# Optimization experiments

Hardware: AMD Instinct MI355X
Metric: run time of the kernel (lower is better)

Reference implementation:

```python
import jax, jax.numpy as jnp
import numpy as np

B, S, HID = 1, 2048, 4096
NH, NKV = 32, 8
HD = HID // NH            # 128
GROUPS = NH // NKV        # 4
ROPE_THETA = 10000.0


def _rope_cos_sin(seq_len, head_dim, dtype=jnp.float32):
    inv_freq = 1.0 / (ROPE_THETA ** (jnp.arange(0, head_dim, 2, dtype=jnp.float32) / head_dim))
    t = jnp.arange(seq_len, dtype=jnp.float32)
    freqs = jnp.outer(t, inv_freq)                      # [S, HD/2]
    emb = jnp.concatenate([freqs, freqs], axis=-1)      # [S, HD]
    return jnp.cos(emb).astype(dtype), jnp.sin(emb).astype(dtype)


def _rotate_half(x):
    x1, x2 = jnp.split(x, 2, axis=-1)
    return jnp.concatenate([-x2, x1], axis=-1)


def _apply_rope(x, cos, sin):
    # x: [B, H, S, HD]; cos/sin: [S, HD] (position_ids = arange(S), no past)
    return x * cos[None, None] + _rotate_half(x) * sin[None, None]


def setup_inputs() -> dict:
    key = jax.random.key(0)
    k1, k2, k3, k4, k5 = jax.random.split(key, 5)
    return {
        "hidden_states": jax.random.normal(k1, (B, S, HID), jnp.float32),
        "Wq": jax.random.normal(k2, (NH * HD, HID), jnp.float32) * 0.02,
        "Wk": jax.random.normal(k3, (NKV * HD, HID), jnp.float32) * 0.02,
        "Wv": jax.random.normal(k4, (NKV * HD, HID), jnp.float32) * 0.02,
        "Wo": jax.random.normal(k5, (HID, NH * HD), jnp.float32) * 0.02,
    }


def reference(hidden_states, Wq, Wk, Wv, Wo):
    bsz, q_len, _ = hidden_states.shape
    # projections (nn.Linear: x @ W.T)
    q = (hidden_states @ Wq.T).reshape(bsz, q_len, NH, HD).transpose(0, 2, 1, 3)   # [B,NH,S,HD]
    k = (hidden_states @ Wk.T).reshape(bsz, q_len, NKV, HD).transpose(0, 2, 1, 3)  # [B,NKV,S,HD]
    v = (hidden_states @ Wv.T).reshape(bsz, q_len, NKV, HD).transpose(0, 2, 1, 3)

    cos, sin = _rope_cos_sin(q_len, HD, hidden_states.dtype)
    q = _apply_rope(q, cos, sin)
    k = _apply_rope(k, cos, sin)

    # GQA: repeat kv heads (repeat_kv / num_key_value_groups)
    k = jnp.repeat(k, GROUPS, axis=1)   # [B,NH,S,HD]
    v = jnp.repeat(v, GROUPS, axis=1)

    scale = 1.0 / jnp.sqrt(jnp.asarray(HD, hidden_states.dtype))
    logits = jnp.einsum('bhqd,bhkd->bhqk', q, k) * scale   # [B,NH,S,S]

    # prefill causal mask (phys_past_len = 0)
    causal = jnp.tril(jnp.ones((q_len, q_len), dtype=bool))
    logits = jnp.where(causal[None, None], logits, jnp.finfo(logits.dtype).min)

    attn = jax.nn.softmax(logits, axis=-1)
    out = jnp.einsum('bhqk,bhkd->bhqd', attn, v)            # [B,NH,S,HD]
    out = out.transpose(0, 2, 1, 3).reshape(bsz, q_len, NH * HD)
    return out @ Wo.T
```

## Files before the change

kernel.cpp:

```cpp
#include <hip/hip_runtime.h>

typedef __bf16 bf16;
typedef __bf16 bf16x4 __attribute__((ext_vector_type(4)));
typedef __bf16 bf16x8 __attribute__((ext_vector_type(8)));
typedef float f32x4 __attribute__((ext_vector_type(4)));

#define S_LEN 2048
#define HID_DIM 4096
#define NH 32
#define NKV 8
#define HD 128
#define QKV_N 6144
#define K_COL 4096
#define V_COL 5120
#define PADV 76

__global__ void cvt_all_kernel(const float* __restrict__ hs, const float* __restrict__ wq,
                               const float* __restrict__ wk, const float* __restrict__ wv,
                               const float* __restrict__ wo, bf16* __restrict__ hsb,
                               bf16* __restrict__ wqkvb, bf16* __restrict__ wob) {
  long i = (long)blockIdx.x * blockDim.x + threadIdx.x;
  const float* src; bf16* dst; long off;
  if (i < 2097152)      { src = hs; dst = hsb;   off = i; }
  else if (i < 6291456) { src = wq; dst = wqkvb; off = i - 2097152; }
  else if (i < 7340032) { src = wk; dst = wqkvb + (long)4096 * 4096 / 4 * 4; off = i - 6291456; dst = wqkvb + (long)4096 * 4096; }
  else if (i < 8388608) { src = wv; dst = wqkvb + (long)5120 * 4096; off = i - 7340032; }
  else                  { src = wo; dst = wob;   off = i - 8388608; }
  float4 v = reinterpret_cast<const float4*>(src)[off];
  bf16x4 o;
  o[0] = (bf16)v.x; o[1] = (bf16)v.y; o[2] = (bf16)v.z; o[3] = (bf16)v.w;
  reinterpret_cast<bf16x4*>(dst)[off] = o;
}

__global__ void rope_table_kernel(float* __restrict__ cost, float* __restrict__ sint) {
  int i = blockIdx.x * blockDim.x + threadIdx.x;
  int s = i >> 6, d = i & 63;
  float inv = expf(-0.14391156831212787f * (float)d);
  float ang = (float)s * inv;
  cost[i] = cosf(ang);
  sint[i] = sinf(ang);
}

__global__ void rope_apply_kernel(bf16* __restrict__ qkv, const float* __restrict__ cost,
                                  const float* __restrict__ sint) {
  int idx = blockIdx.x * blockDim.x + threadIdx.x;
  int s = idx / 320;
  int c = idx - s * 320;
  int g = c >> 3, dc = (c & 7) * 8;
  long base = (long)s * QKV_N + g * 128 + dc;
  bf16x8 x1 = *reinterpret_cast<const bf16x8*>(qkv + base);
  bf16x8 x2 = *reinterpret_cast<const bf16x8*>(qkv + base + 64);
  const float* cp = cost + (s << 6) + dc;
  const float* sp = sint + (s << 6) + dc;
  float4 ca = *reinterpret_cast<const float4*>(cp);
  float4 cb = *reinterpret_cast<const float4*>(cp + 4);
  float4 sa = *reinterpret_cast<const float4*>(sp);
  float4 sb = *reinterpret_cast<const float4*>(sp + 4);
  float co[8] = {ca.x, ca.y, ca.z, ca.w, cb.x, cb.y, cb.z, cb.w};
  float sn[8] = {sa.x, sa.y, sa.z, sa.w, sb.x, sb.y, sb.z, sb.w};
  bf16x8 y1, y2;
#pragma unroll
  for (int e = 0; e < 8; ++e) {
    float a = (float)x1[e], b = (float)x2[e];
    y1[e] = (bf16)(a * co[e] - b * sn[e]);
    y2[e] = (bf16)(b * co[e] + a * sn[e]);
  }
  *reinterpret_cast<bf16x8*>(qkv + base)      = y1;
  *reinterpret_cast<bf16x8*>(qkv + base + 64) = y2;
}

template<typename OutT>
__global__ __launch_bounds__(256, 2) void gemm_bt_kernel(
    const bf16* __restrict__ A, const bf16* __restrict__ B, OutT* __restrict__ C,
    int M, int N, int K) {
  __shared__ __align__(16) bf16 As[128 * 64];
  __shared__ __align__(16) bf16 Bs[128 * 64];

  int nwg = gridDim.x * gridDim.y;
  int bid = blockIdx.y * gridDim.x + blockIdx.x;
  int cpx = nwg >> 3;
  int swz = (bid & 7) * cpx + (bid >> 3);
  int bx = swz % gridDim.x, by = swz / gridDim.x;
  const int n0 = bx * 128, m0 = by * 128;

  const int t = threadIdx.x;
  const int lane = t & 63, w = t >> 6;
  const int wr = w >> 1, wc = w & 1;
  const int lg = lane >> 4, lm = lane & 15;
  f32x4 acc[4][4] = {};

  for (int k0 = 0; k0 < K; k0 += 64) {
    __syncthreads();
#pragma unroll
    for (int i = 0; i < 4; ++i) {
      int c = i * 256 + t;
      int r = c >> 3, jl = c & 7;
      int jg = jl ^ (r & 7);
      const bf16* srcA = A + (long)(m0 + r) * K + k0 + jg * 8;
      __builtin_amdgcn_global_load_lds((const __attribute__((address_space(1))) void*)srcA,
                                       (__attribute__((address_space(3))) void*)(As + c * 8), 16, 0, 0);
      const bf16* srcB = B + (long)(n0 + r) * K + k0 + jg * 8;
      __builtin_amdgcn_global_load_lds((const __attribute__((address_space(1))) void*)srcB,
                                       (__attribute__((address_space(3))) void*)(Bs + c * 8), 16, 0, 0);
    }
    __syncthreads();
#pragma unroll
    for (int ks = 0; ks < 2; ++ks) {
      bf16x8 a[4], b[4];
#pragma unroll
      for (int m = 0; m < 4; ++m) {
        int r = wr * 64 + m * 16 + lm;
        int j = ks * 4 + lg;
        a[m] = *reinterpret_cast<const bf16x8*>(As + r * 64 + ((j ^ (r & 7)) << 3));
      }
#pragma unroll
      for (int n = 0; n < 4; ++n) {
        int r = wc * 64 + n * 16 + lm;
        int j = ks * 4 + lg;
        b[n] = *reinterpret_cast<const bf16x8*>(Bs + r * 64 + ((j ^ (r & 7)) << 3));
      }
#pragma unroll
      for (int m = 0; m < 4; ++m)
#pragma unroll
        for (int n = 0; n < 4; ++n)
          acc[m][n] = __builtin_amdgcn_mfma_f32_16x16x32_bf16(a[m], b[n], acc[m][n], 0, 0, 0);
    }
  }
#pragma unroll
  for (int m = 0; m < 4; ++m) {
    int row = m0 + wr * 64 + m * 16 + lg * 4;
#pragma unroll
    for (int n = 0; n < 4; ++n) {
      int col = n0 + wc * 64 + n * 16 + lm;
#pragma unroll
      for (int r = 0; r < 4; ++r) {
        float v = acc[m][n][r];
        if constexpr (sizeof(OutT) == 4) C[(long)(row + r) * N + col] = v;
        else                             C[(long)(row + r) * N + col] = (bf16)v;
      }
    }
  }
}

__global__ __launch_bounds__(256, 3) void attn_kernel(const bf16* __restrict__ qkv,
                                                      bf16* __restrict__ out) {
  __shared__ __align__(16) bf16 Ks[2][64 * 128];
  __shared__ __align__(16) bf16 Vt[128 * PADV];

  const int bx = blockIdx.x;
  const int qt = 31 - (bx >> 5);
  const int h = bx & 31;
  const int kvh = h >> 2;
  const int q0 = qt * 64;
  const int t = threadIdx.x, lane = t & 63, w = t >> 6;
  const int lg = lane >> 4, lm = lane & 15;
  const int dchunk = t >> 4, kv4 = t & 15;
  const int pcol = ((kv4 >> 3) << 5) | ((kv4 & 3) << 3) | (((kv4 >> 2) & 1) << 2);
  const bf16* kbase = qkv + K_COL + kvh * HD;
  const bf16* vbase = qkv + V_COL + kvh * HD;

  const long qrow = q0 + w * 16 + lm;
  bf16x8 qf[4];
#pragma unroll
  for (int ks = 0; ks < 4; ++ks)
    qf[ks] = *reinterpret_cast<const bf16x8*>(qkv + qrow * QKV_N + h * HD + ks * 32 + lg * 8);

  f32x4 o[8];
#pragma unroll
  for (int i = 0; i < 8; ++i) o[i] = f32x4{0.f, 0.f, 0.f, 0.f};
  float mrow = -1e30f, lrow = 0.f;

  bf16x8 a0, a1, a2, a3;
  {
#pragma unroll
    for (int i = 0; i < 4; ++i) {
      int c = i * 256 + t;
      int r = c >> 4, jl = c & 15;
      int jg = jl ^ (r & 15);
      const bf16* src = kbase + (long)r * QKV_N + jg * 8;
      __builtin_amdgcn_global_load_lds((const __attribute__((address_space(1))) void*)src,
                                       (__attribute__((address_space(3))) void*)(Ks[0] + c * 8), 16, 0, 0);
    }
    const bf16* vs = vbase + (long)(kv4 * 4) * QKV_N + dchunk * 8;
    a0 = *reinterpret_cast<const bf16x8*>(vs);
    a1 = *reinterpret_cast<const bf16x8*>(vs + QKV_N);
    a2 = *reinterpret_cast<const bf16x8*>(vs + 2 * QKV_N);
    a3 = *reinterpret_cast<const bf16x8*>(vs + 3 * QKV_N);
  }

  for (int st = 0; st <= qt; ++st) {
    const int cur = st & 1;
#pragma unroll
    for (int e = 0; e < 8; ++e) {
      bf16x4 pk; pk[0] = a0[e]; pk[1] = a1[e]; pk[2] = a2[e]; pk[3] = a3[e];
      *reinterpret_cast<bf16x4*>(Vt + (dchunk * 8 + e) * PADV + pcol) = pk;
    }
    __syncthreads();

    if (st < qt) {
      const long kv0n = (long)(st + 1) * 64;
#pragma unroll
      for (int i = 0; i < 4; ++i) {
        int c = i * 256 + t;
        int r = c >> 4, jl = c & 15;
        int jg = jl ^ (r & 15);
        const bf16* src = kbase + (kv0n + r) * QKV_N + jg * 8;
        __builtin_amdgcn_global_load_lds((const __attribute__((address_space(1))) void*)src,
                                         (__attribute__((address_space(3))) void*)(Ks[cur ^ 1] + c * 8), 16, 0, 0);
      }
      const bf16* vs = vbase + (kv0n + kv4 * 4) * QKV_N + dchunk * 8;
      a0 = *reinterpret_cast<const bf16x8*>(vs);
      a1 = *reinterpret_cast<const bf16x8*>(vs + QKV_N);
      a2 = *reinterpret_cast<const bf16x8*>(vs + 2 * QKV_N);
      a3 = *reinterpret_cast<const bf16x8*>(vs + 3 * QKV_N);
    }

    f32x4 s[4];
#pragma unroll
    for (int cb = 0; cb < 4; ++cb) s[cb] = f32x4{0.f, 0.f, 0.f, 0.f};
    __builtin_amdgcn_s_setprio(1);
#pragma unroll
    for (int ks = 0; ks < 4; ++ks) {
#pragma unroll
      for (int cb = 0; cb < 4; ++cb) {
        bf16x8 kf = *reinterpret_cast<const bf16x8*>(
            Ks[cur] + (cb * 16 + lm) * 128 + (((ks * 4 + lg) ^ lm) << 3));
        s[cb] = __builtin_amdgcn_mfma_f32_16x16x32_bf16(kf, qf[ks], s[cb], 0, 0, 0);
      }
    }
    __builtin_amdgcn_s_setprio(0);

    const float SC = 0.12751742f;
    const int kv0 = st * 64;
    const int qg = q0 + w * 16 + lm;
    float sl[4][4];
#pragma unroll
    for (int cb = 0; cb < 4; ++cb)
#pragma unroll
      for (int r = 0; r < 4; ++r) {
        float v = s[cb][r] * SC;
        if (st == qt && (kv0 + cb * 16 + lg * 4 + r) > qg) v = -1e30f;
        sl[cb][r] = v;
      }
    float tm = sl[0][0];
#pragma unroll
    for (int cb = 0; cb < 4; ++cb)
#pragma unroll
      for (int r = 0; r < 4; ++r) tm = fmaxf(tm, sl[cb][r]);
    tm = fmaxf(tm, __shfl_xor(tm, 16));
    tm = fmaxf(tm, __shfl_xor(tm, 32));

    if (__any(tm > mrow + 8.f)) {
      float mnew = fmaxf(mrow, tm);
      float alpha = exp2f(mrow - mnew);
      mrow = mnew;
      lrow *= alpha;
      float ar[4];
#pragma unroll
      for (int r = 0; r < 4; ++r)
        ar[r] = __shfl(alpha, (lane & 48) | (lg * 4 + r));
#pragma unroll
      for (int i = 0; i < 8; ++i)
#pragma unroll
        for (int r = 0; r < 4; ++r) o[i][r] *= ar[r];
    }
    float p[4][4];
    float psum = 0.f;
#pragma unroll
    for (int cb = 0; cb < 4; ++cb)
#pragma unroll
      for (int r = 0; r < 4; ++r) {
        p[cb][r] = exp2f(sl[cb][r] - mrow);
        psum += p[cb][r];
      }
    psum += __shfl_xor(psum, 16);
    psum += __shfl_xor(psum, 32);
    lrow += psum;

    bf16x8 pa0, pa1;
#pragma unroll
    for (int r = 0; r < 4; ++r) {
      pa0[r]     = (bf16)p[0][r];
      pa0[4 + r] = (bf16)p[1][r];
      pa1[r]     = (bf16)p[2][r];
      pa1[4 + r] = (bf16)p[3][r];
    }

    __builtin_amdgcn_s_setprio(1);
#pragma unroll
    for (int db = 0; db < 8; ++db) {
      bf16x8 vf0 = *reinterpret_cast<const bf16x8*>(Vt + (db * 16 + lm) * PADV + lg * 8);
      bf16x8 vf1 = *reinterpret_cast<const bf16x8*>(Vt + (db * 16 + lm) * PADV + 32 + lg * 8);
      o[db] = __builtin_amdgcn_mfma_f32_16x16x32_bf16(pa0, vf0, o[db], 0, 0, 0);
      o[db] = __builtin_amdgcn_mfma_f32_16x16x32_bf16(pa1, vf1, o[db], 0, 0, 0);
    }
    __builtin_amdgcn_s_setprio(0);

    if (st < qt) __syncthreads();
  }

  float invr[4];
#pragma unroll
  for (int r = 0; r < 4; ++r)
    invr[r] = 1.0f / __shfl(lrow, (lane & 48) | (lg * 4 + r));
#pragma unroll
  for (int r = 0; r < 4; ++r) {
    long row = q0 + w * 16 + lg * 4 + r;
#pragma unroll
    for (int db = 0; db < 8; ++db)
      out[row * HID_DIM + h * HD + db * 16 + lm] = (bf16)(o[db][r] * invr[r]);
  }
}

extern "C" void kernel_launch(void* const* d_in, const int* in_sizes, int n_in,
                              void* d_out, int out_size, void* d_ws, size_t ws_size,
                              hipStream_t stream) {
  const float* hs = (const float*)d_in[0];
  const float* Wq = (const float*)d_in[1];
  const float* Wk = (const float*)d_in[2];
  const float* Wv = (const float*)d_in[3];
  const float* Wo = (const float*)d_in[4];
  float* out = (float*)d_out;
  char* ws = (char*)d_ws;

  bf16*  hsb   = (bf16*)(ws);
  bf16*  wqkvb = (bf16*)(ws + 16777216);
  bf16*  wob   = (bf16*)(ws + 67108864);
  bf16*  qkv   = (bf16*)(ws + 100663296);
  bf16*  attn  = (bf16*)(ws + 125829120);
  float* cost  = (float*)(ws + 142606336);
  float* sint  = (float*)(ws + 143130624);

  cvt_all_kernel<<<49152, 256, 0, stream>>>(hs, Wq, Wk, Wv, Wo, hsb, wqkvb, wob);
  rope_table_kernel<<<512, 256, 0, stream>>>(cost, sint);
  gemm_bt_kernel<bf16><<<dim3(48, 16), 256, 0, stream>>>(hsb, wqkvb, qkv, 2048, 6144, 4096);
  rope_apply_kernel<<<2560, 256, 0, stream>>>(qkv, cost, sint);
  attn_kernel<<<1024, 256, 0, stream>>>(qkv, attn);
  gemm_bt_kernel<float><<<dim3(32, 16), 256, 0, stream>>>(attn, wob, out, 2048, 4096, 4096);
}
```

Before: 328.8 us.

## Add 256x256 pipelined QKV GEMM and widen attention blocks to 128 query rows

Replaces the QKV projection GEMM with a new 512-thread kernel that uses 256x256 tiles, double-buffered LDS staging with XOR swizzle, grouped block swizzling, and interleaved load/MFMA phases. The attention kernel now handles 128 query rows per block with 8 waves, so each K/V tile loaded into shared memory is reused by twice as many queries, and waves skip tiles that are fully masked. It also cleans up the duplicated destination assignment in the conversion kernel. The new GEMM uses only 192 blocks, which can leave compute units idle, and its hand-placed waitcnt and barrier schedule is easy to get wrong.

```diff
diff --git a/kernel.cpp b/kernel.cpp
--- a/kernel.cpp
+++ b/kernel.cpp
@@ -1,6 +1,7 @@
 #include <hip/hip_runtime.h>
 
 typedef __bf16 bf16;
+typedef __bf16 bf16x2 __attribute__((ext_vector_type(2)));
 typedef __bf16 bf16x4 __attribute__((ext_vector_type(4)));
 typedef __bf16 bf16x8 __attribute__((ext_vector_type(8)));
 typedef float f32x4 __attribute__((ext_vector_type(4)));
@@ -21,11 +22,11 @@
                                bf16* __restrict__ wqkvb, bf16* __restrict__ wob) {
   long i = (long)blockIdx.x * blockDim.x + threadIdx.x;
   const float* src; bf16* dst; long off;
-  if (i < 2097152)      { src = hs; dst = hsb;   off = i; }
-  else if (i < 6291456) { src = wq; dst = wqkvb; off = i - 2097152; }
-  else if (i < 7340032) { src = wk; dst = wqkvb + (long)4096 * 4096 / 4 * 4; off = i - 6291456; dst = wqkvb + (long)4096 * 4096; }
-  else if (i < 8388608) { src = wv; dst = wqkvb + (long)5120 * 4096; off = i - 7340032; }
-  else                  { src = wo; dst = wob;   off = i - 8388608; }
+  if (i < 2097152)      { src = hs; dst = hsb;                          off = i; }
+  else if (i < 6291456) { src = wq; dst = wqkvb;                        off = i - 2097152; }
+  else if (i < 7340032) { src = wk; dst = wqkvb + (long)4096 * 4096;    off = i - 6291456; }
+  else if (i < 8388608) { src = wv; dst = wqkvb + (long)5120 * 4096;    off = i - 7340032; }
+  else                  { src = wo; dst = wob;                          off = i - 8388608; }
   float4 v = reinterpret_cast<const float4*>(src)[off];
   bf16x4 o;
   o[0] = (bf16)v.x; o[1] = (bf16)v.y; o[2] = (bf16)v.z; o[3] = (bf16)v.w;
@@ -142,20 +143,147 @@
   }
 }
 
-__global__ __launch_bounds__(256, 3) void attn_kernel(const bf16* __restrict__ qkv,
+#define STG(buf, mat, kt, half) {                                                        \
+  const bf16* sp_ = (mat) ? Bp : Ap;                                                     \
+  int row0_ = ((mat) ? n0 : m0) + (half) * 128;                                          \
+  int lb_ = (buf) * 32768 + (mat) * 16384 + (half) * 8192;                               \
+  _Pragma("unroll") for (int ii_ = 0; ii_ < 2; ++ii_) {                                  \
+    int c_ = ii_ * 512 + t;                                                              \
+    int r_ = c_ >> 3, jl_ = c_ & 7, jg_ = jl_ ^ (r_ & 7);                                \
+    const bf16* src_ = sp_ + (long)(row0_ + r_) * K + (kt) * 64 + jg_ * 8;               \
+    __builtin_amdgcn_global_load_lds((const __attribute__((address_space(1))) void*)src_,\
+        (__attribute__((address_space(3))) void*)(L + lb_ + c_ * 8), 16, 0, 0);          \
+  } }
+
+#define DSA(ab_, mh) {                                                                   \
+  _Pragma("unroll") for (int mf_ = 0; mf_ < 4; ++mf_)                                    \
+    _Pragma("unroll") for (int ks_ = 0; ks_ < 2; ++ks_) {                                \
+      int R_ = wr * 128 + (mh) * 64 + mf_ * 16 + lm;                                     \
+      aF[mf_][ks_] = *reinterpret_cast<const bf16x8*>(                                   \
+          L + (ab_) + R_ * 64 + (((ks_ * 4 + lg) ^ (R_ & 7)) << 3));                     \
+    } }
+
+#define DSB(bb_, nh, bfr) {                                                              \
+  _Pragma("unroll") for (int nf_ = 0; nf_ < 2; ++nf_)                                    \
+    _Pragma("unroll") for (int ks_ = 0; ks_ < 2; ++ks_) {                                \
+      int R_ = wc * 64 + (nh) * 32 + nf_ * 16 + lm;                                      \
+      bfr[nf_][ks_] = *reinterpret_cast<const bf16x8*>(                                  \
+          L + (bb_) + R_ * 64 + (((ks_ * 4 + lg) ^ (R_ & 7)) << 3));                     \
+    } }
+
+#define MM(mh, nh, bfr) {                                                                \
+  __builtin_amdgcn_s_setprio(1);                                                         \
+  _Pragma("unroll") for (int mf_ = 0; mf_ < 4; ++mf_)                                    \
+    _Pragma("unroll") for (int nf_ = 0; nf_ < 2; ++nf_)                                  \
+      _Pragma("unroll") for (int ks_ = 0; ks_ < 2; ++ks_)                                \
+        acc[(mh) * 4 + mf_][(nh) * 2 + nf_] = __builtin_amdgcn_mfma_f32_16x16x32_bf16(   \
+            aF[mf_][ks_], bfr[nf_][ks_], acc[(mh) * 4 + mf_][(nh) * 2 + nf_], 0, 0, 0);  \
+  __builtin_amdgcn_s_setprio(0); }
+
+#define BAR() __builtin_amdgcn_s_barrier()
+
+__global__ __launch_bounds__(512, 1) void gemm256_kernel(
+    const bf16* __restrict__ Ap, const bf16* __restrict__ Bp, bf16* __restrict__ C,
+    int M, int N, int K) {
+  __shared__ __align__(16) bf16 L[65536];
+
+  int nwg = gridDim.x * gridDim.y;
+  int bid = blockIdx.y * gridDim.x + blockIdx.x;
+  int cpx = nwg >> 3;
+  int swz = (bid & 7) * cpx + (bid >> 3);
+  int bxs = swz % gridDim.x, bys = swz / gridDim.x;
+  const int n0 = bxs * 256, m0 = bys * 256;
+
+  const int t = threadIdx.x;
+  const int lane = t & 63, w = t >> 6;
+  const int wr = w >> 2, wc = w & 3;
+  const int lg = lane >> 4, lm = lane & 15;
+  const int NT = K >> 6;
+
+  f32x4 acc[8][4] = {};
+  bf16x8 aF[4][2], bF0[2][2], bF1[2][2];
+
+  STG(0, 0, 0, 0); STG(0, 0, 0, 1); STG(0, 1, 0, 0); STG(0, 1, 0, 1);
+  STG(1, 1, 1, 0); STG(1, 1, 1, 1);
+  asm volatile("s_waitcnt vmcnt(4)" ::: "memory");
+  BAR();
+
+  for (int I = 0; I < (NT >> 1); ++I) {
+    const int tt = 2 * I;
+    const bool pf = (I < (NT >> 1) - 1);
+    DSA(0, 0); DSB(16384, 0, bF0);
+    STG(1, 0, tt + 1, 0);
+    BAR();
+    MM(0, 0, bF0);
+    BAR();
+    DSB(16384, 1, bF1);
+    STG(1, 0, tt + 1, 1);
+    BAR();
+    MM(0, 1, bF1);
+    BAR();
+    DSA(0, 1);
+    if (pf) STG(0, 1, tt + 2, 0);
+    BAR();
+    MM(1, 0, bF0);
+    BAR();
+    if (pf) STG(0, 1, tt + 2, 1);
+    BAR();
+    MM(1, 1, bF1);
+    if (pf) asm volatile("s_waitcnt vmcnt(4)" ::: "memory");
+    else    asm volatile("s_waitcnt vmcnt(0)" ::: "memory");
+    BAR();
+    DSA(32768, 0); DSB(49152, 0, bF0);
+    if (pf) STG(0, 0, tt + 2, 0);
+    BAR();
+    MM(0, 0, bF0);
+    BAR();
+    DSB(49152, 1, bF1);
+    if (pf) STG(0, 0, tt + 2, 1);
+    BAR();
+    MM(0, 1, bF1);
+    BAR();
+    DSA(32768, 1);
+    if (pf) STG(1, 1, tt + 3, 0);
+    BAR();
+    MM(1, 0, bF0);
+    BAR();
+    if (pf) STG(1, 1, tt + 3, 1);
+    BAR();
+    MM(1, 1, bF1);
+    if (pf) asm volatile("s_waitcnt vmcnt(4)" ::: "memory");
+    else    asm volatile("s_waitcnt vmcnt(0)" ::: "memory");
+    BAR();
+  }
+
+#pragma unroll
+  for (int am = 0; am < 8; ++am) {
+    int row = m0 + wr * 128 + am * 16 + lg * 4;
+#pragma unroll
+    for (int an = 0; an < 4; ++an) {
+      int col = n0 + wc * 64 + an * 16 + lm;
+#pragma unroll
+      for (int rr = 0; rr < 4; ++rr)
+        C[(long)(row + rr) * N + col] = (bf16)acc[am][an][rr];
+    }
+  }
+}
+
+__global__ __launch_bounds__(512, 4) void attn_kernel(const bf16* __restrict__ qkv,
                                                       bf16* __restrict__ out) {
   __shared__ __align__(16) bf16 Ks[2][64 * 128];
   __shared__ __align__(16) bf16 Vt[128 * PADV];
 
   const int bx = blockIdx.x;
-  const int qt = 31 - (bx >> 5);
+  const int qt = 15 - (bx >> 5);
   const int h = bx & 31;
   const int kvh = h >> 2;
-  const int q0 = qt * 64;
+  const int q0 = qt * 128;
   const int t = threadIdx.x, lane = t & 63, w = t >> 6;
   const int lg = lane >> 4, lm = lane & 15;
-  const int dchunk = t >> 4, kv4 = t & 15;
-  const int pcol = ((kv4 >> 3) << 5) | ((kv4 & 3) << 3) | (((kv4 >> 2) & 1) << 2);
+  const int dchunk = t >> 5, kv2 = t & 31;
+  const int kva = kv2 * 2;
+  const int k5 = kva & 31;
+  const int slot = ((kva >> 5) << 5) | (((k5 >> 2) & 3) << 3) | ((k5 >> 4) << 2) | (k5 & 3);
   const bf16* kbase = qkv + K_COL + kvh * HD;
   const bf16* vbase = qkv + V_COL + kvh * HD;
 
@@ -170,133 +298,132 @@
   for (int i = 0; i < 8; ++i) o[i] = f32x4{0.f, 0.f, 0.f, 0.f};
   float mrow = -1e30f, lrow = 0.f;
 
-  bf16x8 a0, a1, a2, a3;
+  bf16x8 a0, a1;
   {
 #pragma unroll
-    for (int i = 0; i < 4; ++i) {
-      int c = i * 256 + t;
+    for (int i = 0; i < 2; ++i) {
+      int c = i * 512 + t;
       int r = c >> 4, jl = c & 15;
       int jg = jl ^ (r & 15);
       const bf16* src = kbase + (long)r * QKV_N + jg * 8;
       __builtin_amdgcn_global_load_lds((const __attribute__((address_space(1))) void*)src,
                                        (__attribute__((address_space(3))) void*)(Ks[0] + c * 8), 16, 0, 0);
     }
-    const bf16* vs = vbase + (long)(kv4 * 4) * QKV_N + dchunk * 8;
+    const bf16* vs = vbase + (long)kva * QKV_N + dchunk * 8;
     a0 = *reinterpret_cast<const bf16x8*>(vs);
     a1 = *reinterpret_cast<const bf16x8*>(vs + QKV_N);
-    a2 = *reinterpret_cast<const bf16x8*>(vs + 2 * QKV_N);
-    a3 = *reinterpret_cast<const bf16x8*>(vs + 3 * QKV_N);
-  }
-
-  for (int st = 0; st <= qt; ++st) {
+  }
+
+  const int nst = 2 * qt + 2;
+  for (int st = 0; st < nst; ++st) {
     const int cur = st & 1;
 #pragma unroll
     for (int e = 0; e < 8; ++e) {
-      bf16x4 pk; pk[0] = a0[e]; pk[1] = a1[e]; pk[2] = a2[e]; pk[3] = a3[e];
-      *reinterpret_cast<bf16x4*>(Vt + (dchunk * 8 + e) * PADV + pcol) = pk;
+      bf16x2 pk; pk[0] = a0[e]; pk[1] = a1[e];
+      *reinterpret_cast<bf16x2*>(Vt + (dchunk * 8 + e) * PADV + slot) = pk;
     }
     __syncthreads();
 
-    if (st < qt) {
+    if (st + 1 < nst) {
       const long kv0n = (long)(st + 1) * 64;
 #pragma unroll
-      for (int i = 0; i < 4; ++i) {
-        int c = i * 256 + t;
+      for (int i = 0; i < 2; ++i) {
+        int c = i * 512 + t;
         int r = c >> 4, jl = c & 15;
         int jg = jl ^ (r & 15);
         const bf16* src = kbase + (kv0n + r) * QKV_N + jg * 8;
         __builtin_amdgcn_global_load_lds((const __attribute__((address_space(1))) void*)src,
                                          (__attribute__((address_space(3))) void*)(Ks[cur ^ 1] + c * 8), 16, 0, 0);
       }
-      const bf16* vs = vbase + (kv0n + kv4 * 4) * QKV_N + dchunk * 8;
+      const bf16* vs = vbase + (kv0n + kva) * QKV_N + dchunk * 8;
       a0 = *reinterpret_cast<const bf16x8*>(vs);
       a1 = *reinterpret_cast<const bf16x8*>(vs + QKV_N);
-      a2 = *reinterpret_cast<const bf16x8*>(vs + 2 * QKV_N);
-      a3 = *reinterpret_cast<const bf16x8*>(vs + 3 * QKV_N);
-    }
-
-    f32x4 s[4];
-#pragma unroll
-    for (int cb = 0; cb < 4; ++cb) s[cb] = f32x4{0.f, 0.f, 0.f, 0.f};
-    __builtin_amdgcn_s_setprio(1);
-#pragma unroll
-    for (int ks = 0; ks < 4; ++ks) {
-#pragma unroll
-      for (int cb = 0; cb < 4; ++cb) {
-        bf16x8 kf = *reinterpret_cast<const bf16x8*>(
-            Ks[cur] + (cb * 16 + lm) * 128 + (((ks * 4 + lg) ^ lm) << 3));
-        s[cb] = __builtin_amdgcn_mfma_f32_16x16x32_bf16(kf, qf[ks], s[cb], 0, 0, 0);
-      }
-    }
-    __builtin_amdgcn_s_setprio(0);
-
-    const float SC = 0.12751742f;
+    }
+
     const int kv0 = st * 64;
     const int qg = q0 + w * 16 + lm;
-    float sl[4][4];
-#pragma unroll
-    for (int cb = 0; cb < 4; ++cb)
+    if (kv0 <= q0 + w * 16 + 15) {
+      f32x4 s[4];
+#pragma unroll
+      for (int cb = 0; cb < 4; ++cb) s[cb] = f32x4{0.f, 0.f, 0.f, 0.f};
+      __builtin_amdgcn_s_setprio(1);
+#pragma unroll
+      for (int ks = 0; ks < 4; ++ks) {
+#pragma unroll
+        for (int cb = 0; cb < 4; ++cb) {
+          bf16x8 kf = *reinterpret_cast<const bf16x8*>(
+              Ks[cur] + (cb * 16 + lm) * 128 + (((ks * 4 + lg) ^ lm) << 3));
+          s[cb] = __builtin_amdgcn_mfma_f32_16x16x32_bf16(kf, qf[ks], s[cb], 0, 0, 0);
+        }
+      }
+      __builtin_amdgcn_s_setprio(0);
+
+      const float SC = 0.12751742f;
+      float sl[4][4];
+#pragma unroll
+      for (int cb = 0; cb < 4; ++cb)
+#pragma unroll
+        for (int r = 0; r < 4; ++r) {
+          float v = s[cb][r] * SC;
+          if (st >= nst - 2 && (kv0 + cb * 16 + lg * 4 + r) > qg) v = -1e30f;
+          sl[cb][r] = v;
+        }
+      float tm = sl[0][0];
+#pragma unroll
+      for (int cb = 0; cb < 4; ++cb)
+#pragma unroll
+        for (int r = 0; r < 4; ++r) tm = fmaxf(tm, sl[cb][r]);
+      tm = fmaxf(tm, __shfl_xor(tm, 16));
+      tm = fmaxf(tm, __shfl_xor(tm, 32));
+
+      if (__any(tm > mrow + 8.f)) {
+        float mnew = fmaxf(mrow, tm);
+        float alpha = exp2f(mrow - mnew);
+        mrow = mnew;
+        lrow *= alpha;
+        float ar[4];
+#pragma unroll
+        for (int r = 0; r < 4; ++r)
+          ar[r] = __shfl(alpha, (lane & 48) | (lg * 4 + r));
+#pragma unroll
+        for (int i = 0; i < 8; ++i)
+#pragma unroll
+          for (int r = 0; r < 4; ++r) o[i][r] *= ar[r];
+      }
+      float p[4][4];
+      float psum = 0.f;
+#pragma unroll
+      for (int cb = 0; cb < 4; ++cb)
+#pragma unroll
+        for (int r = 0; r < 4; ++r) {
+          p[cb][r] = exp2f(sl[cb][r] - mrow);
+          psum += p[cb][r];
+        }
+      psum += __shfl_xor(psum, 16);
+      psum += __shfl_xor(psum, 32);
+      lrow += psum;
+
+      bf16x8 pa0, pa1;
 #pragma unroll
       for (int r = 0; r < 4; ++r) {
-        float v = s[cb][r] * SC;
-        if (st == qt && (kv0 + cb * 16 + lg * 4 + r) > qg) v = -1e30f;
-        sl[cb][r] = v;
-      }
-    float tm = sl[0][0];
-#pragma unroll
-    for (int cb = 0; cb < 4; ++cb)
-#pragma unroll
-      for (int r = 0; r < 4; ++r) tm = fmaxf(tm, sl[cb][r]);
-    tm = fmaxf(tm, __shfl_xor(tm, 16));
-    tm = fmaxf(tm, __shfl_xor(tm, 32));
-
-    if (__any(tm > mrow + 8.f)) {
-      float mnew = fmaxf(mrow, tm);
-      float alpha = exp2f(mrow - mnew);
-      mrow = mnew;
-      lrow *= alpha;
-      float ar[4];
-#pragma unroll
-      for (int r = 0; r < 4; ++r)
-        ar[r] = __shfl(alpha, (lane & 48) | (lg * 4 + r));
-#pragma unroll
-      for (int i = 0; i < 8; ++i)
-#pragma unroll
-        for (int r = 0; r < 4; ++r) o[i][r] *= ar[r];
-    }
-    float p[4][4];
-    float psum = 0.f;
-#pragma unroll
-    for (int cb = 0; cb < 4; ++cb)
-#pragma unroll
-      for (int r = 0; r < 4; ++r) {
-        p[cb][r] = exp2f(sl[cb][r] - mrow);
-        psum += p[cb][r];
-      }
-    psum += __shfl_xor(psum, 16);
-    psum += __shfl_xor(psum, 32);
-    lrow += psum;
-
-    bf16x8 pa0, pa1;
-#pragma unroll
-    for (int r = 0; r < 4; ++r) {
-      pa0[r]     = (bf16)p[0][r];
-      pa0[4 + r] = (bf16)p[1][r];
-      pa1[r]     = (bf16)p[2][r];
-      pa1[4 + r] = (bf16)p[3][r];
-    }
-
-    __builtin_amdgcn_s_setprio(1);
-#pragma unroll
-    for (int db = 0; db < 8; ++db) {
-      bf16x8 vf0 = *reinterpret_cast<const bf16x8*>(Vt + (db * 16 + lm) * PADV + lg * 8);
-      bf16x8 vf1 = *reinterpret_cast<const bf16x8*>(Vt + (db * 16 + lm) * PADV + 32 + lg * 8);
-      o[db] = __builtin_amdgcn_mfma_f32_16x16x32_bf16(pa0, vf0, o[db], 0, 0, 0);
-      o[db] = __builtin_amdgcn_mfma_f32_16x16x32_bf16(pa1, vf1, o[db], 0, 0, 0);
-    }
-    __builtin_amdgcn_s_setprio(0);
-
-    if (st < qt) __syncthreads();
+        pa0[r]     = (bf16)p[0][r];
+        pa0[4 + r] = (bf16)p[1][r];
+        pa1[r]     = (bf16)p[2][r];
+        pa1[4 + r] = (bf16)p[3][r];
+      }
+
+      __builtin_amdgcn_s_setprio(1);
+#pragma unroll
+      for (int db = 0; db < 8; ++db) {
+        bf16x8 vf0 = *reinterpret_cast<const bf16x8*>(Vt + (db * 16 + lm) * PADV + lg * 8);
+        bf16x8 vf1 = *reinterpret_cast<const bf16x8*>(Vt + (db * 16 + lm) * PADV + 32 + lg * 8);
+        o[db] = __builtin_amdgcn_mfma_f32_16x16x32_bf16(pa0, vf0, o[db], 0, 0, 0);
+        o[db] = __builtin_amdgcn_mfma_f32_16x16x32_bf16(pa1, vf1, o[db], 0, 0, 0);
+      }
+      __builtin_amdgcn_s_setprio(0);
+    }
+
+    if (st + 1 < nst) __syncthreads();
   }
 
   float invr[4];
@@ -333,8 +460,8 @@
 
   cvt_all_kernel<<<49152, 256, 0, stream>>>(hs, Wq, Wk, Wv, Wo, hsb, wqkvb, wob);
   rope_table_kernel<<<512, 256, 0, stream>>>(cost, sint);
-  gemm_bt_kernel<bf16><<<dim3(48, 16), 256, 0, stream>>>(hsb, wqkvb, qkv, 2048, 6144, 4096);
+  gemm256_kernel<<<dim3(24, 8), 512, 0, stream>>>(hsb, wqkvb, qkv, 2048, 6144, 4096);
   rope_apply_kernel<<<2560, 256, 0, stream>>>(qkv, cost, sint);
-  attn_kernel<<<1024, 256, 0, stream>>>(qkv, attn);
+  attn_kernel<<<512, 512, 0, stream>>>(qkv, attn);
   gemm_bt_kernel<float><<<dim3(32, 16), 256, 0, stream>>>(attn, wob, out, 2048, 4096, 4096);
 }
```

After: 321.1 us. 1.02x faster.

## Replace GEMMs with 8-wave double-buffered kernel and widen attention query tile

Applied to the files above, without the earlier changes.

Both projection GEMMs move to a 512-thread, 8-wave kernel with 256-row tiles and double-buffered LDS. Global-to-LDS loads for later k-tiles are interleaved between MFMA phases using explicit vmcnt waits and barriers, aiming at more reuse per tile and hidden load latency. The attention kernel now handles 128 query rows per block with 512 threads, shares each K/V tile across twice as many waves, and skips fully masked tiles per wave. This costs more registers and LDS per block, fewer blocks in flight, and a fragile hand-written pipeline schedule.

```diff
diff --git a/kernel.cpp b/kernel.cpp
--- a/kernel.cpp
+++ b/kernel.cpp
@@ -1,6 +1,7 @@
 #include <hip/hip_runtime.h>
 
 typedef __bf16 bf16;
+typedef __bf16 bf16x2 __attribute__((ext_vector_type(2)));
 typedef __bf16 bf16x4 __attribute__((ext_vector_type(4)));
 typedef __bf16 bf16x8 __attribute__((ext_vector_type(8)));
 typedef float f32x4 __attribute__((ext_vector_type(4)));
@@ -21,11 +22,11 @@
                                bf16* __restrict__ wqkvb, bf16* __restrict__ wob) {
   long i = (long)blockIdx.x * blockDim.x + threadIdx.x;
   const float* src; bf16* dst; long off;
-  if (i < 2097152)      { src = hs; dst = hsb;   off = i; }
-  else if (i < 6291456) { src = wq; dst = wqkvb; off = i - 2097152; }
-  else if (i < 7340032) { src = wk; dst = wqkvb + (long)4096 * 4096 / 4 * 4; off = i - 6291456; dst = wqkvb + (long)4096 * 4096; }
-  else if (i < 8388608) { src = wv; dst = wqkvb + (long)5120 * 4096; off = i - 7340032; }
-  else                  { src = wo; dst = wob;   off = i - 8388608; }
+  if (i < 2097152)      { src = hs; dst = hsb;                          off = i; }
+  else if (i < 6291456) { src = wq; dst = wqkvb;                        off = i - 2097152; }
+  else if (i < 7340032) { src = wk; dst = wqkvb + (long)4096 * 4096;    off = i - 6291456; }
+  else if (i < 8388608) { src = wv; dst = wqkvb + (long)5120 * 4096;    off = i - 7340032; }
+  else                  { src = wo; dst = wob;                          off = i - 8388608; }
   float4 v = reinterpret_cast<const float4*>(src)[off];
   bf16x4 o;
   o[0] = (bf16)v.x; o[1] = (bf16)v.y; o[2] = (bf16)v.z; o[3] = (bf16)v.w;
@@ -69,93 +70,134 @@
   *reinterpret_cast<bf16x8*>(qkv + base + 64) = y2;
 }
 
-template<typename OutT>
-__global__ __launch_bounds__(256, 2) void gemm_bt_kernel(
-    const bf16* __restrict__ A, const bf16* __restrict__ B, OutT* __restrict__ C,
+#define STG8(buf, mat, kt, unit) {                                                       \
+    const bf16* sp_ = (mat) ? Bp : Ap;                                                   \
+    int row0_ = ((mat) ? n0 : m0) + (unit) * 64;                                         \
+    int lb_ = (buf) * LBUF + (mat) * 16384 + (unit) * 4096;                              \
+    int r_ = t >> 3, jl_ = t & 7, jg_ = jl_ ^ (r_ & 7);                                  \
+    const bf16* src_ = sp_ + (long)(row0_ + r_) * K + (kt) * 64 + jg_ * 8;               \
+    __builtin_amdgcn_global_load_lds((const __attribute__((address_space(1))) void*)src_,\
+        (__attribute__((address_space(3))) void*)(L + lb_ + t * 8), 16, 0, 0); }
+
+#define DSA8(buf, mh, ks) {                                                              \
+    _Pragma("unroll") for (int mf_ = 0; mf_ < 4; ++mf_) {                                \
+      int R_ = wr * 128 + (mh) * 64 + mf_ * 16 + lm;                                     \
+      aF[mf_] = *reinterpret_cast<const bf16x8*>(                                        \
+          L + (buf) * LBUF + R_ * 64 + ((((ks) * 4 + lg) ^ (R_ & 7)) << 3));             \
+    } }
+
+#define DSB8(buf) {                                                                      \
+    _Pragma("unroll") for (int ks_ = 0; ks_ < 2; ++ks_)                                  \
+      _Pragma("unroll") for (int nf_ = 0; nf_ < NB; ++nf_) {                             \
+        int R_ = wc * (NB * 16) + nf_ * 16 + lm;                                         \
+        bF[ks_][nf_] = *reinterpret_cast<const bf16x8*>(                                 \
+            L + (buf) * LBUF + 16384 + R_ * 64 + (((ks_ * 4 + lg) ^ (R_ & 7)) << 3));    \
+      } }
+
+#define MM8(mh, ks) {                                                                    \
+    __builtin_amdgcn_s_setprio(1);                                                       \
+    _Pragma("unroll") for (int mf_ = 0; mf_ < 4; ++mf_)                                  \
+      _Pragma("unroll") for (int nf_ = 0; nf_ < NB; ++nf_)                               \
+        acc[(mh) * 4 + mf_][nf_] = __builtin_amdgcn_mfma_f32_16x16x32_bf16(              \
+            aF[mf_], bF[ks][nf_], acc[(mh) * 4 + mf_][nf_], 0, 0, 0);                    \
+    __builtin_amdgcn_s_setprio(0); }
+
+#define BAR() __builtin_amdgcn_s_barrier()
+#define WVM(n) asm volatile("s_waitcnt vmcnt(%0)" :: "i"(n) : "memory")
+
+template<int NB, typename OutT>
+__global__ __launch_bounds__(512, 1) void gemm8p_kernel(
+    const bf16* __restrict__ Ap, const bf16* __restrict__ Bp, OutT* __restrict__ C,
     int M, int N, int K) {
-  __shared__ __align__(16) bf16 As[128 * 64];
-  __shared__ __align__(16) bf16 Bs[128 * 64];
+  constexpr int LBUF = 16384 + NB * 4096;
+  __shared__ __align__(16) bf16 L[2 * LBUF];
 
   int nwg = gridDim.x * gridDim.y;
   int bid = blockIdx.y * gridDim.x + blockIdx.x;
   int cpx = nwg >> 3;
   int swz = (bid & 7) * cpx + (bid >> 3);
-  int bx = swz % gridDim.x, by = swz / gridDim.x;
-  const int n0 = bx * 128, m0 = by * 128;
+  int bxs = swz % gridDim.x, bys = swz / gridDim.x;
+  const int n0 = bxs * (NB * 64), m0 = bys * 256;
 
   const int t = threadIdx.x;
   const int lane = t & 63, w = t >> 6;
-  const int wr = w >> 1, wc = w & 1;
+  const int wr = w >> 2, wc = w & 3;
   const int lg = lane >> 4, lm = lane & 15;
-  f32x4 acc[4][4] = {};
-
-  for (int k0 = 0; k0 < K; k0 += 64) {
-    __syncthreads();
-#pragma unroll
-    for (int i = 0; i < 4; ++i) {
-      int c = i * 256 + t;
-      int r = c >> 3, jl = c & 7;
-      int jg = jl ^ (r & 7);
-      const bf16* srcA = A + (long)(m0 + r) * K + k0 + jg * 8;
-      __builtin_amdgcn_global_load_lds((const __attribute__((address_space(1))) void*)srcA,
-                                       (__attribute__((address_space(3))) void*)(As + c * 8), 16, 0, 0);
-      const bf16* srcB = B + (long)(n0 + r) * K + k0 + jg * 8;
-      __builtin_amdgcn_global_load_lds((const __attribute__((address_space(1))) void*)srcB,
-                                       (__attribute__((address_space(3))) void*)(Bs + c * 8), 16, 0, 0);
-    }
-    __syncthreads();
-#pragma unroll
-    for (int ks = 0; ks < 2; ++ks) {
-      bf16x8 a[4], b[4];
-#pragma unroll
-      for (int m = 0; m < 4; ++m) {
-        int r = wr * 64 + m * 16 + lm;
-        int j = ks * 4 + lg;
-        a[m] = *reinterpret_cast<const bf16x8*>(As + r * 64 + ((j ^ (r & 7)) << 3));
-      }
-#pragma unroll
-      for (int n = 0; n < 4; ++n) {
-        int r = wc * 64 + n * 16 + lm;
-        int j = ks * 4 + lg;
-        b[n] = *reinterpret_cast<const bf16x8*>(Bs + r * 64 + ((j ^ (r & 7)) << 3));
-      }
-#pragma unroll
-      for (int m = 0; m < 4; ++m)
-#pragma unroll
-        for (int n = 0; n < 4; ++n)
-          acc[m][n] = __builtin_amdgcn_mfma_f32_16x16x32_bf16(a[m], b[n], acc[m][n], 0, 0, 0);
-    }
-  }
-#pragma unroll
-  for (int m = 0; m < 4; ++m) {
-    int row = m0 + wr * 64 + m * 16 + lg * 4;
-#pragma unroll
-    for (int n = 0; n < 4; ++n) {
-      int col = n0 + wc * 64 + n * 16 + lm;
-#pragma unroll
-      for (int r = 0; r < 4; ++r) {
-        float v = acc[m][n][r];
-        if constexpr (sizeof(OutT) == 4) C[(long)(row + r) * N + col] = v;
-        else                             C[(long)(row + r) * N + col] = (bf16)v;
-      }
-    }
-  }
-}
-
-__global__ __launch_bounds__(256, 3) void attn_kernel(const bf16* __restrict__ qkv,
+  const int NT = K >> 6;
+
+  f32x4 acc[8][NB] = {};
+  bf16x8 aF[4], bF[2][NB];
+
+  STG8(0, 0, 0, 0); STG8(0, 0, 0, 1); STG8(0, 0, 0, 2); STG8(0, 0, 0, 3);
+  STG8(0, 1, 0, 0); if (NB > 1) STG8(0, 1, 0, 1); if (NB > 2) STG8(0, 1, 0, 2);
+  STG8(1, 1, 1, 0); if (NB > 1) STG8(1, 1, 1, 1); if (NB > 2) STG8(1, 1, 1, 2);
+  WVM(NB);
+  BAR();
+
+  for (int I = 0; I < (NT >> 1); ++I) {
+    const int tt = 2 * I;
+    const bool pf = (I < (NT >> 1) - 1);
+    DSA8(0, 0, 0); DSB8(0);
+    STG8(1, 0, tt + 1, 0); STG8(1, 0, tt + 1, 1);
+    BAR(); MM8(0, 0); BAR();
+    DSA8(0, 1, 0);
+    STG8(1, 0, tt + 1, 2); STG8(1, 0, tt + 1, 3);
+    BAR(); MM8(1, 0); BAR();
+    DSA8(0, 0, 1);
+    if (pf) { STG8(0, 1, tt + 2, 0); if (NB > 1) STG8(0, 1, tt + 2, 1); }
+    BAR(); MM8(0, 1); BAR();
+    DSA8(0, 1, 1);
+    if (pf) { if (NB > 2) STG8(0, 1, tt + 2, 2); }
+    BAR(); MM8(1, 1);
+    if (pf) WVM(NB); else WVM(0);
+    BAR();
+    DSA8(1, 0, 0); DSB8(1);
+    if (pf) { STG8(0, 0, tt + 2, 0); STG8(0, 0, tt + 2, 1); }
+    BAR(); MM8(0, 0); BAR();
+    DSA8(1, 1, 0);
+    if (pf) { STG8(0, 0, tt + 2, 2); STG8(0, 0, tt + 2, 3); }
+    BAR(); MM8(1, 0); BAR();
+    DSA8(1, 0, 1);
+    if (pf) { STG8(1, 1, tt + 3, 0); if (NB > 1) STG8(1, 1, tt + 3, 1); }
+    BAR(); MM8(0, 1); BAR();
+    DSA8(1, 1, 1);
+    if (pf) { if (NB > 2) STG8(1, 1, tt + 3, 2); }
+    BAR(); MM8(1, 1);
+    if (pf) WVM(NB); else WVM(0);
+    BAR();
+  }
+
+#pragma unroll
+  for (int am = 0; am < 8; ++am) {
+    int row = m0 + wr * 128 + am * 16 + lg * 4;
+#pragma unroll
+    for (int nf = 0; nf < NB; ++nf) {
+      int col = n0 + wc * (NB * 16) + nf * 16 + lm;
+#pragma unroll
+      for (int rr = 0; rr < 4; ++rr) {
+        if constexpr (sizeof(OutT) == 4) C[(long)(row + rr) * N + col] = acc[am][nf][rr];
+        else                             C[(long)(row + rr) * N + col] = (bf16)acc[am][nf][rr];
+      }
+    }
+  }
+}
+
+__global__ __launch_bounds__(512, 4) void attn_kernel(const bf16* __restrict__ qkv,
                                                       bf16* __restrict__ out) {
   __shared__ __align__(16) bf16 Ks[2][64 * 128];
   __shared__ __align__(16) bf16 Vt[128 * PADV];
 
   const int bx = blockIdx.x;
-  const int qt = 31 - (bx >> 5);
+  const int qt = 15 - (bx >> 5);
   const int h = bx & 31;
   const int kvh = h >> 2;
-  const int q0 = qt * 64;
+  const int q0 = qt * 128;
   const int t = threadIdx.x, lane = t & 63, w = t >> 6;
   const int lg = lane >> 4, lm = lane & 15;
-  const int dchunk = t >> 4, kv4 = t & 15;
-  const int pcol = ((kv4 >> 3) << 5) | ((kv4 & 3) << 3) | (((kv4 >> 2) & 1) << 2);
+  const int dchunk = t >> 5, kv2 = t & 31;
+  const int kva = kv2 * 2;
+  const int k5 = kva & 31;
+  const int slot = ((kva >> 5) << 5) | (((k5 >> 2) & 3) << 3) | ((k5 >> 4) << 2) | (k5 & 3);
   const bf16* kbase = qkv + K_COL + kvh * HD;
   const bf16* vbase = qkv + V_COL + kvh * HD;
 
@@ -170,133 +212,132 @@
   for (int i = 0; i < 8; ++i) o[i] = f32x4{0.f, 0.f, 0.f, 0.f};
   float mrow = -1e30f, lrow = 0.f;
 
-  bf16x8 a0, a1, a2, a3;
+  bf16x8 a0, a1;
   {
 #pragma unroll
-    for (int i = 0; i < 4; ++i) {
-      int c = i * 256 + t;
+    for (int i = 0; i < 2; ++i) {
+      int c = i * 512 + t;
       int r = c >> 4, jl = c & 15;
       int jg = jl ^ (r & 15);
       const bf16* src = kbase + (long)r * QKV_N + jg * 8;
       __builtin_amdgcn_global_load_lds((const __attribute__((address_space(1))) void*)src,
                                        (__attribute__((address_space(3))) void*)(Ks[0] + c * 8), 16, 0, 0);
     }
-    const bf16* vs = vbase + (long)(kv4 * 4) * QKV_N + dchunk * 8;
+    const bf16* vs = vbase + (long)kva * QKV_N + dchunk * 8;
     a0 = *reinterpret_cast<const bf16x8*>(vs);
     a1 = *reinterpret_cast<const bf16x8*>(vs + QKV_N);
-    a2 = *reinterpret_cast<const bf16x8*>(vs + 2 * QKV_N);
-    a3 = *reinterpret_cast<const bf16x8*>(vs + 3 * QKV_N);
-  }
-
-  for (int st = 0; st <= qt; ++st) {
+  }
+
+  const int nst = 2 * qt + 2;
+  for (int st = 0; st < nst; ++st) {
     const int cur = st & 1;
 #pragma unroll
     for (int e = 0; e < 8; ++e) {
-      bf16x4 pk; pk[0] = a0[e]; pk[1] = a1[e]; pk[2] = a2[e]; pk[3] = a3[e];
-      *reinterpret_cast<bf16x4*>(Vt + (dchunk * 8 + e) * PADV + pcol) = pk;
+      bf16x2 pk; pk[0] = a0[e]; pk[1] = a1[e];
+      *reinterpret_cast<bf16x2*>(Vt + (dchunk * 8 + e) * PADV + slot) = pk;
     }
     __syncthreads();
 
-    if (st < qt) {
+    if (st + 1 < nst) {
       const long kv0n = (long)(st + 1) * 64;
 #pragma unroll
-      for (int i = 0; i < 4; ++i) {
-        int c = i * 256 + t;
+      for (int i = 0; i < 2; ++i) {
+        int c = i * 512 + t;
         int r = c >> 4, jl = c & 15;
         int jg = jl ^ (r & 15);
         const bf16* src = kbase + (kv0n + r) * QKV_N + jg * 8;
         __builtin_amdgcn_global_load_lds((const __attribute__((address_space(1))) void*)src,
                                          (__attribute__((address_space(3))) void*)(Ks[cur ^ 1] + c * 8), 16, 0, 0);
       }
-      const bf16* vs = vbase + (kv0n + kv4 * 4) * QKV_N + dchunk * 8;
+      const bf16* vs = vbase + (kv0n + kva) * QKV_N + dchunk * 8;
       a0 = *reinterpret_cast<const bf16x8*>(vs);
       a1 = *reinterpret_cast<const bf16x8*>(vs + QKV_N);
-      a2 = *reinterpret_cast<const bf16x8*>(vs + 2 * QKV_N);
-      a3 = *reinterpret_cast<const bf16x8*>(vs + 3 * QKV_N);
-    }
-
-    f32x4 s[4];
-#pragma unroll
-    for (int cb = 0; cb < 4; ++cb) s[cb] = f32x4{0.f, 0.f, 0.f, 0.f};
-    __builtin_amdgcn_s_setprio(1);
-#pragma unroll
-    for (int ks = 0; ks < 4; ++ks) {
-#pragma unroll
-      for (int cb = 0; cb < 4; ++cb) {
-        bf16x8 kf = *reinterpret_cast<const bf16x8*>(
-            Ks[cur] + (cb * 16 + lm) * 128 + (((ks * 4 + lg) ^ lm) << 3));
-        s[cb] = __builtin_amdgcn_mfma_f32_16x16x32_bf16(kf, qf[ks], s[cb], 0, 0, 0);
-      }
-    }
-    __builtin_amdgcn_s_setprio(0);
-
-    const float SC = 0.12751742f;
+    }
+
     const int kv0 = st * 64;
     const int qg = q0 + w * 16 + lm;
-    float sl[4][4];
-#pragma unroll
-    for (int cb = 0; cb < 4; ++cb)
+    if (kv0 <= q0 + w * 16 + 15) {
+      f32x4 s[4];
+#pragma unroll
+      for (int cb = 0; cb < 4; ++cb) s[cb] = f32x4{0.f, 0.f, 0.f, 0.f};
+      __builtin_amdgcn_s_setprio(1);
+#pragma unroll
+      for (int ks = 0; ks < 4; ++ks) {
+#pragma unroll
+        for (int cb = 0; cb < 4; ++cb) {
+          bf16x8 kf = *reinterpret_cast<const bf16x8*>(
+              Ks[cur] + (cb * 16 + lm) * 128 + (((ks * 4 + lg) ^ lm) << 3));
+          s[cb] = __builtin_amdgcn_mfma_f32_16x16x32_bf16(kf, qf[ks], s[cb], 0, 0, 0);
+        }
+      }
+      __builtin_amdgcn_s_setprio(0);
+
+      const float SC = 0.12751742f;
+      float sl[4][4];
+#pragma unroll
+      for (int cb = 0; cb < 4; ++cb)
+#pragma unroll
+        for (int r = 0; r < 4; ++r) {
+          float v = s[cb][r] * SC;
+          if (st >= nst - 2 && (kv0 + cb * 16 + lg * 4 + r) > qg) v = -1e30f;
+          sl[cb][r] = v;
+        }
+      float tm = sl[0][0];
+#pragma unroll
+      for (int cb = 0; cb < 4; ++cb)
+#pragma unroll
+        for (int r = 0; r < 4; ++r) tm = fmaxf(tm, sl[cb][r]);
+      tm = fmaxf(tm, __shfl_xor(tm, 16));
+      tm = fmaxf(tm, __shfl_xor(tm, 32));
+
+      if (__any(tm > mrow + 8.f)) {
+        float mnew = fmaxf(mrow, tm);
+        float alpha = exp2f(mrow - mnew);
+        mrow = mnew;
+        lrow *= alpha;
+        float ar[4];
+#pragma unroll
+        for (int r = 0; r < 4; ++r)
+          ar[r] = __shfl(alpha, (lane & 48) | (lg * 4 + r));
+#pragma unroll
+        for (int i = 0; i < 8; ++i)
+#pragma unroll
+          for (int r = 0; r < 4; ++r) o[i][r] *= ar[r];
+      }
+      float p[4][4];
+      float psum = 0.f;
+#pragma unroll
+      for (int cb = 0; cb < 4; ++cb)
+#pragma unroll
+        for (int r = 0; r < 4; ++r) {
+          p[cb][r] = exp2f(sl[cb][r] - mrow);
+          psum += p[cb][r];
+        }
+      psum += __shfl_xor(psum, 16);
+      psum += __shfl_xor(psum, 32);
+      lrow += psum;
+
+      bf16x8 pa0, pa1;
 #pragma unroll
       for (int r = 0; r < 4; ++r) {
-        float v = s[cb][r] * SC;
-        if (st == qt && (kv0 + cb * 16 + lg * 4 + r) > qg) v = -1e30f;
-        sl[cb][r] = v;
-      }
-    float tm = sl[0][0];
-#pragma unroll
-    for (int cb = 0; cb < 4; ++cb)
-#pragma unroll
-      for (int r = 0; r < 4; ++r) tm = fmaxf(tm, sl[cb][r]);
-    tm = fmaxf(tm, __shfl_xor(tm, 16));
-    tm = fmaxf(tm, __shfl_xor(tm, 32));
-
-    if (__any(tm > mrow + 8.f)) {
-      float mnew = fmaxf(mrow, tm);
-      float alpha = exp2f(mrow - mnew);
-      mrow = mnew;
-      lrow *= alpha;
-      float ar[4];
-#pragma unroll
-      for (int r = 0; r < 4; ++r)
-        ar[r] = __shfl(alpha, (lane & 48) | (lg * 4 + r));
-#pragma unroll
-      for (int i = 0; i < 8; ++i)
-#pragma unroll
-        for (int r = 0; r < 4; ++r) o[i][r] *= ar[r];
-    }
-    float p[4][4];
-    float psum = 0.f;
-#pragma unroll
-    for (int cb = 0; cb < 4; ++cb)
-#pragma unroll
-      for (int r = 0; r < 4; ++r) {
-        p[cb][r] = exp2f(sl[cb][r] - mrow);
-        psum += p[cb][r];
-      }
-    psum += __shfl_xor(psum, 16);
-    psum += __shfl_xor(psum, 32);
-    lrow += psum;
-
-    bf16x8 pa0, pa1;
-#pragma unroll
-    for (int r = 0; r < 4; ++r) {
-      pa0[r]     = (bf16)p[0][r];
-      pa0[4 + r] = (bf16)p[1][r];
-      pa1[r]     = (bf16)p[2][r];
-      pa1[4 + r] = (bf16)p[3][r];
-    }
-
-    __builtin_amdgcn_s_setprio(1);
-#pragma unroll
-    for (int db = 0; db < 8; ++db) {
-      bf16x8 vf0 = *reinterpret_cast<const bf16x8*>(Vt + (db * 16 + lm) * PADV + lg * 8);
-      bf16x8 vf1 = *reinterpret_cast<const bf16x8*>(Vt + (db * 16 + lm) * PADV + 32 + lg * 8);
-      o[db] = __builtin_amdgcn_mfma_f32_16x16x32_bf16(pa0, vf0, o[db], 0, 0, 0);
-      o[db] = __builtin_amdgcn_mfma_f32_16x16x32_bf16(pa1, vf1, o[db], 0, 0, 0);
-    }
-    __builtin_amdgcn_s_setprio(0);
-
-    if (st < qt) __syncthreads();
+        pa0[r]     = (bf16)p[0][r];
+        pa0[4 + r] = (bf16)p[1][r];
+        pa1[r]     = (bf16)p[2][r];
+        pa1[4 + r] = (bf16)p[3][r];
+      }
+
+      __builtin_amdgcn_s_setprio(1);
+#pragma unroll
+      for (int db = 0; db < 8; ++db) {
+        bf16x8 vf0 = *reinterpret_cast<const bf16x8*>(Vt + (db * 16 + lm) * PADV + lg * 8);
+        bf16x8 vf1 = *reinterpret_cast<const bf16x8*>(Vt + (db * 16 + lm) * PADV + 32 + lg * 8);
+        o[db] = __builtin_amdgcn_mfma_f32_16x16x32_bf16(pa0, vf0, o[db], 0, 0, 0);
+        o[db] = __builtin_amdgcn_mfma_f32_16x16x32_bf16(pa1, vf1, o[db], 0, 0, 0);
+      }
+      __builtin_amdgcn_s_setprio(0);
+    }
+
+    if (st + 1 < nst) __syncthreads();
   }
 
   float invr[4];
@@ -333,8 +374,8 @@
 
   cvt_all_kernel<<<49152, 256, 0, stream>>>(hs, Wq, Wk, Wv, Wo, hsb, wqkvb, wob);
   rope_table_kernel<<<512, 256, 0, stream>>>(cost, sint);
-  gemm_bt_kernel<bf16><<<dim3(48, 16), 256, 0, stream>>>(hsb, wqkvb, qkv, 2048, 6144, 4096);
+  gemm8p_kernel<3, bf16><<<dim3(32, 8), 512, 0, stream>>>(hsb, wqkvb, qkv, 2048, 6144, 4096);
   rope_apply_kernel<<<2560, 256, 0, stream>>>(qkv, cost, sint);
-  attn_kernel<<<1024, 256, 0, stream>>>(qkv, attn);
-  gemm_bt_kernel<float><<<dim3(32, 16), 256, 0, stream>>>(attn, wob, out, 2048, 4096, 4096);
-}
+  attn_kernel<<<512, 512, 0, stream>>>(qkv, attn);
+  gemm8p_kernel<2, float><<<dim3(32, 8), 512, 0, stream>>>(attn, wob, out, 2048, 4096, 4096);
+}
```

Result: faster. 310.7 us (-5.5%).
